# Kernel tuning notes

Measured on AMD Instinct MI355X. Metric: run time of the kernel, lower is better.

The kernel has to match this reference:

```python
import jax, jax.numpy as jnp
import numpy as np

N_ROI = 400
N_GRAPHS = 256
N = N_ROI * N_GRAPHS        # 102400 total nodes (stacked graphs)
E = N * 32                  # 3276800 edges, avg degree 32
T = 64                      # n_timepoints (in_channels of conv1)
H = 32                      # hidden channels of conv1/conv2
BS = 16                     # batch_size init arg = out_channels of conv3
N_CLASSES = 9


def setup_inputs() -> dict:
    key = jax.random.key(0)
    ks = jax.random.split(key, 20)
    s = 0.05
    p = {
        "x": jax.random.normal(ks[0], (N, T), jnp.float32),
        "edge_index": jax.random.randint(ks[1], (2, E), 0, N, dtype=jnp.int32),
        "edge_weight": jax.random.uniform(ks[2], (E,), jnp.float32),
        # ChebConv K=2: two bias-free linears + shared bias per layer
        "W1_0": jax.random.normal(ks[3], (T, H), jnp.float32) * s,
        "W1_1": jax.random.normal(ks[4], (T, H), jnp.float32) * s,
        "b1": jnp.zeros((H,), jnp.float32),
        "W2_0": jax.random.normal(ks[5], (H, H), jnp.float32) * s,
        "W2_1": jax.random.normal(ks[6], (H, H), jnp.float32) * s,
        "b2": jnp.zeros((H,), jnp.float32),
        "W3_0": jax.random.normal(ks[7], (H, BS), jnp.float32) * s,
        "W3_1": jax.random.normal(ks[8], (H, BS), jnp.float32) * s,
        "b3": jnp.zeros((BS,), jnp.float32),
        "fc1_w": jax.random.normal(ks[9], (N_ROI * BS, 256), jnp.float32) * s,
        "fc1_b": jnp.zeros((256,), jnp.float32),
        "fc2_w": jax.random.normal(ks[10], (256, 128), jnp.float32) * s,
        "fc2_b": jnp.zeros((128,), jnp.float32),
        "fc3_w": jax.random.normal(ks[11], (128, N_CLASSES), jnp.float32) * s,
        "fc3_b": jnp.zeros((N_CLASSES,), jnp.float32),
    }
    return p


def reference(x, edge_index, edge_weight, W1_0, W1_1, b1, W2_0, W2_1, b2,
              W3_0, W3_1, b3, fc1_w, fc1_b, fc2_w, fc2_b, fc3_w, fc3_b):
    src, dst = edge_index[0], edge_index[1]
    n = x.shape[0]
    # sym-normalized scaled Laplacian (lambda_max=2): Lhat = -D^-1/2 A D^-1/2
    deg = jax.ops.segment_sum(edge_weight, src, num_segments=n)
    deg_safe = jnp.where(deg > 0, deg, 1.0)
    dinv = jnp.where(deg > 0, jax.lax.rsqrt(deg_safe), 0.0)
    lapw = -(dinv[src] * edge_weight * dinv[dst])  # [E]

    def cheb(h, W0, W1, b):
        # K=2: Tx0 = h, Tx1 = Lhat @ h (gather-scatter over edges)
        tx1 = jax.ops.segment_sum(lapw[:, None] * h[src], dst, num_segments=n)
        return h @ W0 + tx1 @ W1 + b

    h = jax.nn.relu(cheb(x, W1_0, W1_1, b1))     # [N, 32]
    h = jax.nn.relu(cheb(h, W2_0, W2_1, b2))     # [N, 32]
    h = jax.nn.relu(cheb(h, W3_0, W3_1, b3))     # [N, 16]
    # global_mean_pool with batch=arange(N) is identity; reshape to graphs
    h = h.reshape(-1, N_ROI * BS)                # [256, 6400]
    h = h @ fc1_w + fc1_b                        # dropout is eval-mode identity
    h = h @ fc2_w + fc2_b
    return h @ fc3_w + fc3_b                     # [256, 9]
```

## Files before the change

### kernel.cpp

```cpp
#include <hip/hip_runtime.h>

#define NN   102400
#define NE   3276800
#define TT   64
#define HH   32
#define BSC  16
#define NG   256
#define NC   9
#define F1   256
#define F2   128
#define FIN  6400

#define NBUCK 200
#define CAP   18432
#define TILE  8192


__global__ __launch_bounds__(256) void k_init(int* __restrict__ scur,
                                              int* __restrict__ dcur) {
    int t = threadIdx.x;
    if (t < NBUCK) { scur[t] = t * CAP; dcur[t] = t * CAP; }
}

template<int MODE>
__global__ __launch_bounds__(256) void k_part(const int* __restrict__ src,
                                              const int* __restrict__ dst,
                                              const float* __restrict__ ew,
                                              int* __restrict__ gcur,
                                              int2* __restrict__ outbuf) {
    __shared__ int hist[256];
    __shared__ int base[256];
    __shared__ int cur[256];
    __shared__ int gpos[256];
    __shared__ int2 stage[TILE];
    __shared__ unsigned char bkt[TILE];

    int t = threadIdx.x;
    int e0 = blockIdx.x * TILE;

    hist[t] = 0;
    __syncthreads();
#pragma unroll
    for (int i = 0; i < TILE / 256; ++i) {
        int e = e0 + i * 256 + t;
        int key = MODE ? dst[e] : src[e];
        atomicAdd(&hist[key >> 9], 1);
    }
    __syncthreads();
    int h = hist[t];
    base[t] = h;
    __syncthreads();
    for (int off = 1; off < 256; off <<= 1) {
        int add = (t >= off) ? base[t - off] : 0;
        __syncthreads();
        base[t] += add;
        __syncthreads();
    }
    int excl = base[t] - h;
    __syncthreads();
    base[t] = excl;
    cur[t] = excl;
    __syncthreads();
#pragma unroll
    for (int i = 0; i < TILE / 256; ++i) {
        int e = e0 + i * 256 + t;
        int s = src[e];
        int w = __float_as_int(ew[e]);
        int key, pack;
        if (MODE) { int d = dst[e]; key = d; pack = (s << 9) | (d & 511); }
        else      { key = s; pack = s & 511; }
        int b = key >> 9;
        int p = atomicAdd(&cur[b], 1);
        stage[p] = make_int2(pack, w);
        bkt[p] = (unsigned char)b;
    }
    __syncthreads();
    if (t < NBUCK && h > 0) gpos[t] = atomicAdd(&gcur[t], h);
    __syncthreads();
#pragma unroll
    for (int i = 0; i < TILE / 256; ++i) {
        int p = i * 256 + t;
        int b = bkt[p];
        outbuf[gpos[b] + (p - base[b])] = stage[p];
    }
}


__global__ __launch_bounds__(512) void k_deg2(const int* __restrict__ scur,
                                              const int2* __restrict__ sbuck,
                                              float* __restrict__ dinv) {
    __shared__ float acc[512];
    int b = blockIdx.x, t = threadIdx.x;
    acc[t] = 0.f;
    __syncthreads();
    int lo = b * CAP, hi = scur[b];
    for (int j = lo + t; j < hi; j += 512) {
        int2 e = sbuck[j];
        atomicAdd(&acc[e.x], __int_as_float(e.y));
    }
    __syncthreads();
    float v = acc[t];
    dinv[b * 512 + t] = v > 0.f ? rsqrtf(v) : 0.f;
}


__global__ __launch_bounds__(512) void k_fin(const int* __restrict__ dcur,
                                             const int2* __restrict__ dbuck,
                                             const float* __restrict__ dinv,
                                             int2* __restrict__ edata,
                                             int* __restrict__ rowbeg,
                                             int* __restrict__ rowend) {
    __shared__ float dl[512];
    __shared__ int cnt[512];
    __shared__ int base[512];
    __shared__ int cur[512];
    int b = blockIdx.x, t = threadIdx.x;
    dl[t] = dinv[b * 512 + t];
    cnt[t] = 0;
    __syncthreads();
    int lo = b * CAP, hi = dcur[b];
    for (int j = lo + t; j < hi; j += 512)
        atomicAdd(&cnt[dbuck[j].x & 511], 1);
    __syncthreads();
    int h = cnt[t];
    base[t] = h;
    __syncthreads();
    for (int off = 1; off < 512; off <<= 1) {
        int add = (t >= off) ? base[t - off] : 0;
        __syncthreads();
        base[t] += add;
        __syncthreads();
    }
    int beg = lo + base[t] - h;
    rowbeg[b * 512 + t] = beg;
    rowend[b * 512 + t] = beg + h;
    cur[t] = beg;
    __syncthreads();
    for (int j = lo + t; j < hi; j += 512) {
        int2 e = dbuck[j];
        int dlow = e.x & 511;
        int s = e.x >> 9;
        float lw = -dinv[s] * __int_as_float(e.y) * dl[dlow];
        int slot = atomicAdd(&cur[dlow], 1);
        edata[slot] = make_int2(s, __float_as_int(lw));
    }
}

template<int CIN, int COUT>
__global__ __launch_bounds__(256) void k_dual_gemm(const float* __restrict__ in,
                                                   const float* __restrict__ W0,
                                                   const float* __restrict__ W1,
                                                   float* __restrict__ o0,
                                                   float* __restrict__ o1) {
    int node = blockIdx.x * 256 + threadIdx.x;
    const float* row = in + (size_t)node * CIN;
    float a0[COUT], a1[COUT];
#pragma unroll
    for (int c = 0; c < COUT; ++c) { a0[c] = 0.f; a1[c] = 0.f; }
    for (int k = 0; k < CIN; ++k) {
        float xv = row[k];
#pragma unroll
        for (int c = 0; c < COUT; ++c) {
            a0[c] = fmaf(xv, W0[k * COUT + c], a0[c]);
            a1[c] = fmaf(xv, W1[k * COUT + c], a1[c]);
        }
    }
#pragma unroll
    for (int c = 0; c < COUT; ++c) {
        o0[(size_t)node * COUT + c] = a0[c];
        o1[(size_t)node * COUT + c] = a1[c];
    }
}

template<int C>
__global__ __launch_bounds__(256) void k_gather(const int* __restrict__ rowbeg,
                                                const int* __restrict__ rowend,
                                                const int2* __restrict__ edata,
                                                const float* __restrict__ xw,
                                                const float* __restrict__ a,
                                                const float* __restrict__ bias,
                                                float* __restrict__ out) {
    constexpr int L = C / 2;
    constexpr int NPB = 256 / L;
    int tid = threadIdx.x;
    int g = tid / L;
    int lane = tid % L;
    int node = blockIdx.x * NPB + g;
    int start = rowbeg[node], end = rowend[node];
    const float2* xw2 = (const float2*)xw;
    float accx = 0.f, accy = 0.f;
    for (int j = start; j < end; j += 16) {
        unsigned long long p[16];
        float2 v[16];
#pragma unroll
        for (int u = 0; u < 16; ++u) {
            int jj = j + u;
            int idx = jj < end ? jj : end - 1;
            p[u] = __builtin_nontemporal_load((const unsigned long long*)(edata + idx));
        }
#pragma unroll
        for (int u = 0; u < 16; ++u) {
            int s = (int)(unsigned)(p[u] & 0xffffffffu);
            v[u] = xw2[(size_t)s * L + lane];
        }
#pragma unroll
        for (int u = 0; u < 16; ++u) {
            float w = (j + u < end) ? __int_as_float((int)(p[u] >> 32)) : 0.f;
            accx = fmaf(w, v[u].x, accx);
            accy = fmaf(w, v[u].y, accy);
        }
    }
    float2 av = ((const float2*)a)[(size_t)node * L + lane];
    float2 bv = ((const float2*)bias)[lane];
    float rx = av.x + accx + bv.x;
    float ry = av.y + accy + bv.y;
    float2 r;
    r.x = rx > 0.f ? rx : 0.f;
    r.y = ry > 0.f ? ry : 0.f;
    ((float2*)out)[(size_t)node * L + lane] = r;
}

__global__ __launch_bounds__(256) void k_w23(const float* __restrict__ fc2w,
                                             const float* __restrict__ fc3w,
                                             float* __restrict__ w23) {
    int gid = blockIdx.x * 256 + threadIdx.x;
    if (gid >= F1 * NC) return;
    int r = gid / NC, c = gid % NC;
    float acc = 0.f;
    for (int j = 0; j < F2; ++j) acc = fmaf(fc2w[r * F2 + j], fc3w[j * NC + c], acc);
    w23[gid] = acc;
}

__global__ __launch_bounds__(64) void k_bc(const float* __restrict__ fc1b,
                                           const float* __restrict__ fc2b,
                                           const float* __restrict__ fc3b,
                                           const float* __restrict__ fc3w,
                                           const float* __restrict__ w23,
                                           float* __restrict__ bc) {
    int c = threadIdx.x;
    if (c >= NC) return;
    float acc = fc3b[c];
    for (int k = 0; k < F1; ++k) acc = fmaf(fc1b[k], w23[k * NC + c], acc);
    for (int j = 0; j < F2; ++j) acc = fmaf(fc2b[j], fc3w[j * NC + c], acc);
    bc[c] = acc;
}

__global__ __launch_bounds__(256) void k_t1(const float* __restrict__ fc1w,
                                            const float* __restrict__ fc2w,
                                            float* __restrict__ t1) {
    int c = threadIdx.x & 127;
    int rh = threadIdx.x >> 7;
    int r0 = blockIdx.x * 16 + rh;
    float acc[8];
#pragma unroll
    for (int rr = 0; rr < 8; ++rr) acc[rr] = 0.f;
    for (int k = 0; k < F1; ++k) {
        float wv = fc2w[k * F2 + c];
#pragma unroll
        for (int rr = 0; rr < 8; ++rr)
            acc[rr] = fmaf(fc1w[(r0 + rr * 2) * F1 + k], wv, acc[rr]);
    }
#pragma unroll
    for (int rr = 0; rr < 8; ++rr) t1[(r0 + rr * 2) * F2 + c] = acc[rr];
}

__global__ __launch_bounds__(256) void k_wc(const float* __restrict__ t1,
                                            const float* __restrict__ fc3w,
                                            float* __restrict__ wc) {
    int gid = blockIdx.x * 256 + threadIdx.x;
    int r = gid >> 4, c = gid & 15;
    if (c >= NC) return;
    float acc = 0.f;
    for (int j = 0; j < F2; ++j) acc = fmaf(t1[r * F2 + j], fc3w[j * NC + c], acc);
    wc[r * NC + c] = acc;
}

__global__ __launch_bounds__(256) void k_out(const float* __restrict__ h3,
                                             const float* __restrict__ wc,
                                             const float* __restrict__ bc,
                                             float* __restrict__ out) {
    __shared__ float red[256 * 10];
    int g = blockIdx.x, tid = threadIdx.x;
    float acc[NC];
#pragma unroll
    for (int c = 0; c < NC; ++c) acc[c] = 0.f;
    for (int k = tid; k < FIN; k += 256) {
        float hv = h3[(size_t)g * FIN + k];
#pragma unroll
        for (int c = 0; c < NC; ++c) acc[c] = fmaf(hv, wc[k * NC + c], acc[c]);
    }
#pragma unroll
    for (int c = 0; c < NC; ++c) red[tid * 10 + c] = acc[c];
    __syncthreads();
    for (int s = 128; s > 0; s >>= 1) {
        if (tid < s) {
#pragma unroll
            for (int c = 0; c < NC; ++c) red[tid * 10 + c] += red[(tid + s) * 10 + c];
        }
        __syncthreads();
    }
    if (tid < NC) out[g * NC + tid] = red[tid] + bc[tid];
}


extern "C" void kernel_launch(void* const* d_in, const int* in_sizes, int n_in,
                              void* d_out, int out_size, void* d_ws, size_t ws_size,
                              hipStream_t stream) {
    const float* x    = (const float*)d_in[0];
    const int*   ei   = (const int*)d_in[1];
    const float* ew   = (const float*)d_in[2];
    const float* W1_0 = (const float*)d_in[3];
    const float* W1_1 = (const float*)d_in[4];
    const float* b1   = (const float*)d_in[5];
    const float* W2_0 = (const float*)d_in[6];
    const float* W2_1 = (const float*)d_in[7];
    const float* b2   = (const float*)d_in[8];
    const float* W3_0 = (const float*)d_in[9];
    const float* W3_1 = (const float*)d_in[10];
    const float* b3   = (const float*)d_in[11];
    const float* fc1w = (const float*)d_in[12];
    const float* fc1b = (const float*)d_in[13];
    const float* fc2w = (const float*)d_in[14];
    const float* fc2b = (const float*)d_in[15];
    const float* fc3w = (const float*)d_in[16];
    const float* fc3b = (const float*)d_in[17];
    float* out = (float*)d_out;
    float* ws  = (float*)d_ws;

    const int* src = ei;
    const int* dst = ei + NE;

    const size_t REG = (size_t)NBUCK * CAP;
    float* dinv  = ws;
    int2*  dbuck = (int2*)(dinv + NN);
    int2*  sbuck = dbuck + REG;
    int2*  edata = sbuck;
    float* D     = (float*)(sbuck + REG);
    int*   rowbeg = (int*)(D + (size_t)NN * HH);
    int*   rowend = rowbeg + NN;
    int*   scur   = rowend + NN;
    int*   dcur   = scur + ((NBUCK + 1) & ~1);
    float* w23    = (float*)(dcur + ((NBUCK + 1) & ~1));
    float* bc     = w23 + F1 * NC;

    float* A = (float*)dbuck;
    float* B = A + (size_t)NN * HH;

    k_init<<<1, 256, 0, stream>>>(scur, dcur);
    k_part<0><<<NE / TILE, 256, 0, stream>>>(src, dst, ew, scur, sbuck);
    k_part<1><<<NE / TILE, 256, 0, stream>>>(src, dst, ew, dcur, dbuck);
    k_deg2<<<NBUCK, 512, 0, stream>>>(scur, sbuck, dinv);
    k_fin<<<NBUCK, 512, 0, stream>>>(dcur, dbuck, dinv, edata, rowbeg, rowend);

    k_dual_gemm<TT, HH><<<NN / 256, 256, 0, stream>>>(x, W1_0, W1_1, A, B);
    k_gather<HH><<<NN / 16, 256, 0, stream>>>(rowbeg, rowend, edata, B, A, b1, D);

    k_dual_gemm<HH, HH><<<NN / 256, 256, 0, stream>>>(D, W2_0, W2_1, A, B);
    k_gather<HH><<<NN / 16, 256, 0, stream>>>(rowbeg, rowend, edata, B, A, b2, D);

    k_dual_gemm<HH, BSC><<<NN / 256, 256, 0, stream>>>(D, W3_0, W3_1, A, B);
    k_gather<BSC><<<NN / 32, 256, 0, stream>>>(rowbeg, rowend, edata, B, A, b3, D);

    k_w23<<<(F1 * NC + 255) / 256, 256, 0, stream>>>(fc2w, fc3w, w23);
    k_bc<<<1, 64, 0, stream>>>(fc1b, fc2b, fc3b, fc3w, w23, bc);
    float* T1 = A;
    k_t1<<<FIN / 16, 256, 0, stream>>>(fc1w, fc2w, T1);
    float* Wc = B;
    k_wc<<<FIN * 16 / 256, 256, 0, stream>>>(T1, fc3w, Wc);
    k_out<<<NG, 256, 0, stream>>>(D, Wc, bc, out);
}
```

Baseline: 672.7 us.

## Fold symmetric normalization into GEMM and gather epilogues instead of edge weights

Edge weights are no longer pre-multiplied by dinv[src]*dinv[dst] in k_fin, which removes a random dinv gather per edge. Instead the GEMM scales its Tx1 output by dinv[src node], and the gather multiplies the aggregated sum by -dinv[dst]. The GEMM now uses float4 loads and stores, the gather loop goes from a 16-wide padded unroll with nontemporal loads to an 8-wide unroll plus a scalar tail, and the partition tile size is halved. The dinv scaling is redone in every layer rather than once, which adds a little arithmetic.

```diff
diff --git a/kernel.cpp b/kernel.cpp
--- a/kernel.cpp
+++ b/kernel.cpp
@@ -13,7 +13,7 @@
 
 #define NBUCK 200
 #define CAP   18432
-#define TILE  8192
+#define TILE  4096
 
 
 __global__ __launch_bounds__(256) void k_init(int* __restrict__ scur,
@@ -106,16 +106,13 @@
 
 __global__ __launch_bounds__(512) void k_fin(const int* __restrict__ dcur,
                                              const int2* __restrict__ dbuck,
-                                             const float* __restrict__ dinv,
                                              int2* __restrict__ edata,
                                              int* __restrict__ rowbeg,
                                              int* __restrict__ rowend) {
-    __shared__ float dl[512];
     __shared__ int cnt[512];
     __shared__ int base[512];
     __shared__ int cur[512];
     int b = blockIdx.x, t = threadIdx.x;
-    dl[t] = dinv[b * 512 + t];
     cnt[t] = 0;
     __syncthreads();
     int lo = b * CAP, hi = dcur[b];
@@ -138,11 +135,8 @@
     __syncthreads();
     for (int j = lo + t; j < hi; j += 512) {
         int2 e = dbuck[j];
-        int dlow = e.x & 511;
-        int s = e.x >> 9;
-        float lw = -dinv[s] * __int_as_float(e.y) * dl[dlow];
-        int slot = atomicAdd(&cur[dlow], 1);
-        edata[slot] = make_int2(s, __float_as_int(lw));
+        int slot = atomicAdd(&cur[e.x & 511], 1);
+        edata[slot] = make_int2(e.x >> 9, e.y);
     }
 }
 
@@ -150,25 +144,35 @@
 __global__ __launch_bounds__(256) void k_dual_gemm(const float* __restrict__ in,
                                                    const float* __restrict__ W0,
                                                    const float* __restrict__ W1,
+                                                   const float* __restrict__ dinv,
                                                    float* __restrict__ o0,
                                                    float* __restrict__ o1) {
     int node = blockIdx.x * 256 + threadIdx.x;
-    const float* row = in + (size_t)node * CIN;
+    const float4* row4 = (const float4*)(in + (size_t)node * CIN);
     float a0[COUT], a1[COUT];
 #pragma unroll
     for (int c = 0; c < COUT; ++c) { a0[c] = 0.f; a1[c] = 0.f; }
-    for (int k = 0; k < CIN; ++k) {
-        float xv = row[k];
-#pragma unroll
-        for (int c = 0; c < COUT; ++c) {
-            a0[c] = fmaf(xv, W0[k * COUT + c], a0[c]);
-            a1[c] = fmaf(xv, W1[k * COUT + c], a1[c]);
+    for (int k4 = 0; k4 < CIN / 4; ++k4) {
+        float4 x4 = row4[k4];
+        float xs[4] = {x4.x, x4.y, x4.z, x4.w};
+#pragma unroll
+        for (int j = 0; j < 4; ++j) {
+            int k = 4 * k4 + j;
+#pragma unroll
+            for (int c = 0; c < COUT; ++c) {
+                a0[c] = fmaf(xs[j], W0[k * COUT + c], a0[c]);
+                a1[c] = fmaf(xs[j], W1[k * COUT + c], a1[c]);
+            }
         }
     }
-#pragma unroll
-    for (int c = 0; c < COUT; ++c) {
-        o0[(size_t)node * COUT + c] = a0[c];
-        o1[(size_t)node * COUT + c] = a1[c];
+    float dv = dinv[node];
+    float4* p0 = (float4*)(o0 + (size_t)node * COUT);
+    float4* p1 = (float4*)(o1 + (size_t)node * COUT);
+#pragma unroll
+    for (int c4 = 0; c4 < COUT / 4; ++c4) {
+        p0[c4] = make_float4(a0[4 * c4], a0[4 * c4 + 1], a0[4 * c4 + 2], a0[4 * c4 + 3]);
+        p1[c4] = make_float4(a1[4 * c4] * dv, a1[4 * c4 + 1] * dv,
+                             a1[4 * c4 + 2] * dv, a1[4 * c4 + 3] * dv);
     }
 }
 
@@ -179,6 +183,7 @@
                                                 const float* __restrict__ xw,
                                                 const float* __restrict__ a,
                                                 const float* __restrict__ bias,
+                                                const float* __restrict__ dinv,
                                                 float* __restrict__ out) {
     constexpr int L = C / 2;
     constexpr int NPB = 256 / L;
@@ -189,31 +194,33 @@
     int start = rowbeg[node], end = rowend[node];
     const float2* xw2 = (const float2*)xw;
     float accx = 0.f, accy = 0.f;
-    for (int j = start; j < end; j += 16) {
-        unsigned long long p[16];
-        float2 v[16];
-#pragma unroll
-        for (int u = 0; u < 16; ++u) {
-            int jj = j + u;
-            int idx = jj < end ? jj : end - 1;
-            p[u] = __builtin_nontemporal_load((const unsigned long long*)(edata + idx));
-        }
-#pragma unroll
-        for (int u = 0; u < 16; ++u) {
-            int s = (int)(unsigned)(p[u] & 0xffffffffu);
-            v[u] = xw2[(size_t)s * L + lane];
-        }
-#pragma unroll
-        for (int u = 0; u < 16; ++u) {
-            float w = (j + u < end) ? __int_as_float((int)(p[u] >> 32)) : 0.f;
+    int j = start;
+    for (; j + 7 < end; j += 8) {
+        int2 e[8];
+        float2 v[8];
+#pragma unroll
+        for (int u = 0; u < 8; ++u) e[u] = edata[j + u];
+#pragma unroll
+        for (int u = 0; u < 8; ++u) v[u] = xw2[(size_t)e[u].x * L + lane];
+#pragma unroll
+        for (int u = 0; u < 8; ++u) {
+            float w = __int_as_float(e[u].y);
             accx = fmaf(w, v[u].x, accx);
             accy = fmaf(w, v[u].y, accy);
         }
     }
+    for (; j < end; ++j) {
+        int2 e0 = edata[j];
+        float2 v0 = xw2[(size_t)e0.x * L + lane];
+        float w = __int_as_float(e0.y);
+        accx = fmaf(w, v0.x, accx);
+        accy = fmaf(w, v0.y, accy);
+    }
+    float dv = dinv[node];
     float2 av = ((const float2*)a)[(size_t)node * L + lane];
     float2 bv = ((const float2*)bias)[lane];
-    float rx = av.x + accx + bv.x;
-    float ry = av.y + accy + bv.y;
+    float rx = av.x - dv * accx + bv.x;
+    float ry = av.y - dv * accy + bv.y;
     float2 r;
     r.x = rx > 0.f ? rx : 0.f;
     r.y = ry > 0.f ? ry : 0.f;
@@ -350,16 +357,16 @@
     k_part<0><<<NE / TILE, 256, 0, stream>>>(src, dst, ew, scur, sbuck);
     k_part<1><<<NE / TILE, 256, 0, stream>>>(src, dst, ew, dcur, dbuck);
     k_deg2<<<NBUCK, 512, 0, stream>>>(scur, sbuck, dinv);
-    k_fin<<<NBUCK, 512, 0, stream>>>(dcur, dbuck, dinv, edata, rowbeg, rowend);
-
-    k_dual_gemm<TT, HH><<<NN / 256, 256, 0, stream>>>(x, W1_0, W1_1, A, B);
-    k_gather<HH><<<NN / 16, 256, 0, stream>>>(rowbeg, rowend, edata, B, A, b1, D);
-
-    k_dual_gemm<HH, HH><<<NN / 256, 256, 0, stream>>>(D, W2_0, W2_1, A, B);
-    k_gather<HH><<<NN / 16, 256, 0, stream>>>(rowbeg, rowend, edata, B, A, b2, D);
-
-    k_dual_gemm<HH, BSC><<<NN / 256, 256, 0, stream>>>(D, W3_0, W3_1, A, B);
-    k_gather<BSC><<<NN / 32, 256, 0, stream>>>(rowbeg, rowend, edata, B, A, b3, D);
+    k_fin<<<NBUCK, 512, 0, stream>>>(dcur, dbuck, edata, rowbeg, rowend);
+
+    k_dual_gemm<TT, HH><<<NN / 256, 256, 0, stream>>>(x, W1_0, W1_1, dinv, A, B);
+    k_gather<HH><<<NN / 16, 256, 0, stream>>>(rowbeg, rowend, edata, B, A, b1, dinv, D);
+
+    k_dual_gemm<HH, HH><<<NN / 256, 256, 0, stream>>>(D, W2_0, W2_1, dinv, A, B);
+    k_gather<HH><<<NN / 16, 256, 0, stream>>>(rowbeg, rowend, edata, B, A, b2, dinv, D);
+
+    k_dual_gemm<HH, BSC><<<NN / 256, 256, 0, stream>>>(D, W3_0, W3_1, dinv, A, B);
+    k_gather<BSC><<<NN / 32, 256, 0, stream>>>(rowbeg, rowend, edata, B, A, b3, dinv, D);
 
     k_w23<<<(F1 * NC + 255) / 256, 256, 0, stream>>>(fc2w, fc3w, w23);
     k_bc<<<1, 64, 0, stream>>>(fc1b, fc2b, fc3b, fc3w, w23, bc);
```

Result: faster. 570.1 us (-15.2%).
